# Performance work log

Measured on AMD Instinct MI355X. Metric: run time of the kernel, lower is better.

## Reference

```python
import jax, jax.numpy as jnp
import numpy as np

RADIUS = 3.0  # suppression radius in meters (init kwarg `radius`)


def _radius_nms(x, y, valid, radius):
    """Greedy radius NMS over points in index order.
    x, y: [N] coordinates; valid: [N] bool (point belongs to this class).
    Returns keep mask [N]: point kept iff valid and not within `radius` of
    any previously kept point.
    """
    N = x.shape[0]
    r2 = radius * radius

    def step(supp, i):
        keep = valid[i] & jnp.logical_not(supp[i])
        d2 = (x - x[i]) ** 2 + (y - y[i]) ** 2  # [N]
        supp = supp | (keep & (d2 <= r2))
        return supp, keep

    _, keeps = jax.lax.scan(step, jnp.zeros(N, dtype=bool), jnp.arange(N))
    return keeps


def setup_inputs() -> dict:
    key = jax.random.key(0)
    k1, k2 = jax.random.split(key)
    B, C, W, H, CL = 4, 4, 64, 128, 5
    segmented_channels = jax.random.normal(k1, (B, C, W, H), dtype=jnp.float32)
    # lidar channels 0,1 are x,y point coordinates (meters); scale for realism
    lidar = jax.random.normal(k2, (B, CL, W, H), dtype=jnp.float32) * 30.0
    return {"segmented_channels": segmented_channels, "lidar": lidar}


def reference(segmented_channels, lidar):
    B, C, W, H = segmented_channels.shape
    N = W * H
    # val, ind = segmented_channels.max(dim=1) -> per-pixel predicted class
    ind = jnp.argmax(segmented_channels, axis=1).reshape(B, N)  # [B, N] int
    x = lidar[:, 0].reshape(B, N)  # [B, N]
    y = lidar[:, 1].reshape(B, N)
    # classes 1 .. C-1 (class 0 = background, skipped in the loop)
    classes = jnp.arange(1, C)
    valid = ind[:, None, :] == classes[None, :, None]  # [B, C-1, N] bool
    # vmap greedy NMS over classes, then over batch (x,y shared across classes)
    nms_c = jax.vmap(_radius_nms, in_axes=(None, None, 0, None))
    nms_bc = jax.vmap(nms_c, in_axes=(0, 0, 0, None))
    keep = nms_bc(x, y, valid, RADIUS)  # [B, C-1, N] bool
    # dense (padded) stand-in for the ragged per-class kept point lists:
    # kept coordinates where keep, zeros elsewhere
    coords = jnp.stack([x, y], axis=-1)  # [B, N, 2]
    kept_coords = coords[:, None, :, :] * keep[..., None].astype(coords.dtype)  # [B, C-1, N, 2]
    return kept_coords, keep
```

## Files before the change

### kernel.cpp

```cpp
#include <hip/hip_runtime.h>
#include <cstdint>


#define NPTS 8192
#define CAP  2304
#define R2C  9.0f
#define GW   56
#define GORG 117.6f
#define GINV 0.23809524f
#define GMAXC 55.0f
#define SENT 3.0e37f

__global__ __launch_bounds__(1024) void radius_nms_kernel(
    const float* __restrict__ seg,
    const float* __restrict__ lidar,
    float* __restrict__ out)
{
#pragma clang fp contract(off)
    const int bx   = blockIdx.x;
    const int b    = bx / 3;
    const int cls  = (bx % 3) + 1;
    const int tid  = threadIdx.x;
    const int lane = tid & 63;
    const int wv   = tid >> 6;

    __shared__ float2 xy[CAP];
    __shared__ unsigned short cellA[CAP];
    __shared__ unsigned long long keptW[CAP / 64];
    __shared__ int waveTot[16];
    __shared__ float2 gslot[GW * GW * 4];
    __shared__ unsigned int cnt32[(GW * GW + 3) / 4];

    float* out0 = out + (size_t)bx * NPTS * 2;
    float* out1 = out + 196608 + (size_t)bx * NPTS;

    const float4 z4 = make_float4(0.f, 0.f, 0.f, 0.f);
    float4* o04 = (float4*)out0;
    float4* o14 = (float4*)out1;
    for (int i = tid; i < NPTS / 2; i += 1024) o04[i] = z4;
    for (int i = tid; i < NPTS / 4; i += 1024) o14[i] = z4;
    const float2 s2 = make_float2(SENT, SENT);
    for (int i = tid; i < GW * GW * 4; i += 1024) gslot[i] = s2;
    for (int i = tid; i < (GW * GW + 3) / 4; i += 1024) cnt32[i] = 0u;

    const float* segb = seg + (size_t)b * 4 * NPTS;
    const float* lx   = lidar + (size_t)b * 5 * NPTS;
    const float* ly   = lx + NPTS;

    const int n0 = tid * 8;
    const float4 a0 = *(const float4*)(segb + n0);
    const float4 a1 = *(const float4*)(segb + n0 + 4);
    const float4 b0 = *(const float4*)(segb + NPTS + n0);
    const float4 b1 = *(const float4*)(segb + NPTS + n0 + 4);
    const float4 c0 = *(const float4*)(segb + 2 * NPTS + n0);
    const float4 c1 = *(const float4*)(segb + 2 * NPTS + n0 + 4);
    const float4 d0 = *(const float4*)(segb + 3 * NPTS + n0);
    const float4 d1 = *(const float4*)(segb + 3 * NPTS + n0 + 4);
    const float4 xv0 = *(const float4*)(lx + n0);
    const float4 xv1 = *(const float4*)(lx + n0 + 4);
    const float4 yv0 = *(const float4*)(ly + n0);
    const float4 yv1 = *(const float4*)(ly + n0 + 4);

    const float v0[8] = {a0.x,a0.y,a0.z,a0.w, a1.x,a1.y,a1.z,a1.w};
    const float v1[8] = {b0.x,b0.y,b0.z,b0.w, b1.x,b1.y,b1.z,b1.w};
    const float v2[8] = {c0.x,c0.y,c0.z,c0.w, c1.x,c1.y,c1.z,c1.w};
    const float v3[8] = {d0.x,d0.y,d0.z,d0.w, d1.x,d1.y,d1.z,d1.w};
    const float px[8] = {xv0.x,xv0.y,xv0.z,xv0.w, xv1.x,xv1.y,xv1.z,xv1.w};
    const float py[8] = {yv0.x,yv0.y,yv0.z,yv0.w, yv1.x,yv1.y,yv1.z,yv1.w};

    int flags = 0, cnt = 0;
#pragma unroll
    for (int k = 0; k < 8; ++k) {
        int bi = 0; float bv = v0[k];
        if (v1[k] > bv) { bv = v1[k]; bi = 1; }
        if (v2[k] > bv) { bv = v2[k]; bi = 2; }
        if (v3[k] > bv) { bv = v3[k]; bi = 3; }
        if (bi == cls) { flags |= (1 << k); ++cnt; }
    }

    int v = cnt;
    for (int off = 1; off < 64; off <<= 1) {
        int nv = __shfl_up(v, off, 64);
        if (lane >= off) v += nv;
    }
    if (lane == 63) waveTot[wv] = v;
    __syncthreads();
    if (wv == 0) {
        int t = (lane < 16) ? waveTot[lane] : 0;
        for (int off = 1; off < 16; off <<= 1) {
            int nt = __shfl_up(t, off, 64);
            if (lane >= off) t += nt;
        }
        if (lane < 16) waveTot[lane] = t;
    }
    __syncthreads();

    int M = waveTot[15];
    if (M > CAP) M = CAP;
    const int rank0 = ((wv == 0) ? 0 : waveTot[wv - 1]) + v - cnt;
    int base = rank0;
#pragma unroll
    for (int k = 0; k < 8; ++k) {
        if (flags & (1 << k)) {
            if (base < CAP) {
                xy[base] = make_float2(px[k], py[k]);
                float fx = floorf((px[k] + GORG) * GINV);
                fx = fminf(fmaxf(fx, 0.0f), GMAXC);
                float fy = floorf((py[k] + GORG) * GINV);
                fy = fminf(fmaxf(fy, 0.0f), GMAXC);
                cellA[base] = (unsigned short)(((int)fy << 8) | (int)fx);
            }
            ++base;
        }
    }
    __syncthreads();

    if (wv == 0) {
        const int ntiles = (M + 63) >> 6;
        const int packSent = (55 << 8) | 55;

        float qx = 3.0e38f, qy = 3.0e38f;
        int cc = packSent;
        if (lane < M) {
            float2 q = xy[lane]; qx = q.x; qy = q.y;
            cc = cellA[lane];
        }

        for (int t = 0; t < ntiles; ++t) {
            const int ts = t << 6;

            float qxN = 3.0e38f, qyN = 3.0e38f;
            int ccN = packSent;
            {
                const int p2 = ts + 64 + lane;
                if (p2 < M) {
                    float2 q = xy[p2]; qxN = q.x; qyN = q.y;
                    ccN = cellA[p2];
                }
            }

            const int cx = cc & 0xFF, cy = cc >> 8;
            const int cxm = (cx > 0) ? cx - 1 : 0;
            const int cxp = (cx < GW - 1) ? cx + 1 : GW - 1;
            const int rm  = ((cy > 0) ? cy - 1 : 0) * GW;
            const int r0  = cy * GW;
            const int rp  = ((cy < GW - 1) ? cy + 1 : GW - 1) * GW;
            const int cLin = r0 + cx;
            const int c9[9] = { rm + cxm, rm + cx, rm + cxp,
                                r0 + cxm, cLin,    r0 + cxp,
                                rp + cxm, rp + cx, rp + cxp };

            float mm = 1.0e30f;
#pragma unroll
            for (int i = 0; i < 9; ++i) {
                const int sb = c9[i] * 4;
                const float2 s0 = gslot[sb];
                const float2 s1 = gslot[sb + 1];
                const float2 s2r = gslot[sb + 2];
                const float2 s3 = gslot[sb + 3];
                float dx, dy;
                dx = qx - s0.x; dy = qy - s0.y; const float e0 = dx * dx + dy * dy;
                dx = qx - s1.x; dy = qy - s1.y; const float e1 = dx * dx + dy * dy;
                dx = qx - s2r.x; dy = qy - s2r.y; const float e2 = dx * dx + dy * dy;
                dx = qx - s3.x; dy = qy - s3.y; const float e3 = dx * dx + dy * dy;
                const float cm = fminf(fminf(e0, e1), fminf(e2, e3));
                mm = fminf(mm, cm);
            }
            const bool sup = (mm <= R2C);

            int cntT = M - ts; if (cntT > 64) cntT = 64;
            const unsigned long long tm =
                (cntT >= 64) ? ~0ull : ((1ull << cntT) - 1ull);
            unsigned long long alive = __ballot(!sup) & tm;
            unsigned long long keepm = 0ull;
            while (alive) {
                const int l1 = __builtin_ctzll(alive);
                const unsigned long long rest = alive & (alive - 1ull);
                const int l2 =
                    __builtin_ctzll(rest | 0x8000000000000000ull);
                const float x1 = __int_as_float(
                    __builtin_amdgcn_readlane(__float_as_int(qx), l1));
                const float y1 = __int_as_float(
                    __builtin_amdgcn_readlane(__float_as_int(qy), l1));
                const float x2 = __int_as_float(
                    __builtin_amdgcn_readlane(__float_as_int(qx), l2));
                const float y2 = __int_as_float(
                    __builtin_amdgcn_readlane(__float_as_int(qy), l2));
                const float dxa = qx - x1, dya = qy - y1;
                const float dxb = qx - x2, dyb = qy - y2;
                const unsigned long long b1 =
                    __ballot((dxa * dxa + dya * dya) <= R2C);
                const unsigned long long b2 =
                    __ballot((dxb * dxb + dyb * dyb) <= R2C);
                keepm |= 1ull << l1;
                alive &= ~b1;
                if (rest != 0ull && ((b1 >> l2) & 1ull) == 0ull) {
                    keepm |= 1ull << l2;
                    alive &= ~b2;
                }
            }
            if (lane == 0) keptW[t] = keepm;

            if ((keepm >> lane) & 1ull) {
                const unsigned sh = 8u * (unsigned)(cLin & 3);
                unsigned old = atomicAdd(&cnt32[cLin >> 2], 1u << sh);
                unsigned mc = (old >> sh) & 0xFFu;
                if (mc < 4u) gslot[cLin * 4 + (int)mc] = make_float2(qx, qy);
            }

            qx = qxN; qy = qyN; cc = ccN;
        }
    }
    __syncthreads();

    int j = rank0;
#pragma unroll
    for (int k = 0; k < 8; ++k) {
        if (flags & (1 << k)) {
            if (j < M && ((keptW[j >> 6] >> (j & 63)) & 1ull)) {
                const int n = n0 + k;
                out0[2 * n]     = px[k];
                out0[2 * n + 1] = py[k];
                out1[n]         = 1.0f;
            }
            ++j;
        }
    }
}

extern "C" void kernel_launch(void* const* d_in, const int* in_sizes, int n_in,
                              void* d_out, int out_size, void* d_ws, size_t ws_size,
                              hipStream_t stream) {
    const float* seg   = (const float*)d_in[0];
    const float* lidar = (const float*)d_in[1];
    float* out = (float*)d_out;
    radius_nms_kernel<<<dim3(12), dim3(1024), 0, stream>>>(seg, lidar, out);
}
```

Measured before the change: 122.4 us.

## Split radius NMS into prep, single-wave NMS, and scatter kernels

Splits the monolithic kernel into three launches. The first does the argmax, compaction and cell binning and also zeroes the output across 72 extra blocks. The second runs the serial greedy NMS in a single 64-thread wave per (batch, class) with a shared-memory grid. The third scatters the kept points. The goal is to move output zeroing and the 1024-thread block overhead off the serial NMS critical path. In exchange it adds two kernel launches and a global workspace round trip, and it reverts the two-at-a-time ballot loop to one leader per iteration. The fallback keeps the old kernel when no workspace is provided.

```diff
diff --git a/kernel.cpp b/kernel.cpp
--- a/kernel.cpp
+++ b/kernel.cpp
@@ -11,37 +11,33 @@
 #define GMAXC 55.0f
 #define SENT 3.0e37f
 
-__global__ __launch_bounds__(1024) void radius_nms_kernel(
+#define WS_STRIDE 32768
+#define WS_XY     0
+#define WS_CELL   18432
+#define WS_OIDX   23040
+#define WS_KEPT   27648
+#define WS_M      27936
+#define WS_NEED   (12 * WS_STRIDE)
+
+__global__ __launch_bounds__(1024) void k1_prep(
     const float* __restrict__ seg,
     const float* __restrict__ lidar,
-    float* __restrict__ out)
+    float* __restrict__ out,
+    char* __restrict__ ws)
 {
 #pragma clang fp contract(off)
-    const int bx   = blockIdx.x;
-    const int b    = bx / 3;
-    const int cls  = (bx % 3) + 1;
-    const int tid  = threadIdx.x;
+    const int blk = blockIdx.x;
+    const int tid = threadIdx.x;
+    if (blk >= 12) {
+        ((float4*)out)[(size_t)(blk - 12) * 1024 + tid] =
+            make_float4(0.f, 0.f, 0.f, 0.f);
+        return;
+    }
+    const int b    = blk / 3;
+    const int cls  = (blk % 3) + 1;
     const int lane = tid & 63;
     const int wv   = tid >> 6;
-
-    __shared__ float2 xy[CAP];
-    __shared__ unsigned short cellA[CAP];
-    __shared__ unsigned long long keptW[CAP / 64];
     __shared__ int waveTot[16];
-    __shared__ float2 gslot[GW * GW * 4];
-    __shared__ unsigned int cnt32[(GW * GW + 3) / 4];
-
-    float* out0 = out + (size_t)bx * NPTS * 2;
-    float* out1 = out + 196608 + (size_t)bx * NPTS;
-
-    const float4 z4 = make_float4(0.f, 0.f, 0.f, 0.f);
-    float4* o04 = (float4*)out0;
-    float4* o14 = (float4*)out1;
-    for (int i = tid; i < NPTS / 2; i += 1024) o04[i] = z4;
-    for (int i = tid; i < NPTS / 4; i += 1024) o14[i] = z4;
-    const float2 s2 = make_float2(SENT, SENT);
-    for (int i = tid; i < GW * GW * 4; i += 1024) gslot[i] = s2;
-    for (int i = tid; i < (GW * GW + 3) / 4; i += 1024) cnt32[i] = 0u;
 
     const float* segb = seg + (size_t)b * 4 * NPTS;
     const float* lx   = lidar + (size_t)b * 5 * NPTS;
@@ -97,6 +93,244 @@
 
     int M = waveTot[15];
     if (M > CAP) M = CAP;
+
+    char* wsp = ws + (size_t)blk * WS_STRIDE;
+    float2* wxy = (float2*)(wsp + WS_XY);
+    unsigned short* wcell = (unsigned short*)(wsp + WS_CELL);
+    unsigned short* woidx = (unsigned short*)(wsp + WS_OIDX);
+    if (tid == 0) *(int*)(wsp + WS_M) = M;
+
+    int base = ((wv == 0) ? 0 : waveTot[wv - 1]) + v - cnt;
+#pragma unroll
+    for (int k = 0; k < 8; ++k) {
+        if (flags & (1 << k)) {
+            if (base < CAP) {
+                wxy[base] = make_float2(px[k], py[k]);
+                float fx = floorf((px[k] + GORG) * GINV);
+                fx = fminf(fmaxf(fx, 0.0f), GMAXC);
+                float fy = floorf((py[k] + GORG) * GINV);
+                fy = fminf(fmaxf(fy, 0.0f), GMAXC);
+                wcell[base] = (unsigned short)(((int)fy << 8) | (int)fx);
+                woidx[base] = (unsigned short)(n0 + k);
+            }
+            ++base;
+        }
+    }
+}
+
+__global__ __launch_bounds__(64) void k2_nms(char* __restrict__ ws)
+{
+#pragma clang fp contract(off)
+    const int p    = blockIdx.x;
+    const int lane = threadIdx.x;
+
+    char* wsp = ws + (size_t)p * WS_STRIDE;
+    const float2* wxy = (const float2*)(wsp + WS_XY);
+    const unsigned short* wcell = (const unsigned short*)(wsp + WS_CELL);
+    unsigned long long* wkept = (unsigned long long*)(wsp + WS_KEPT);
+    const int M = *(const int*)(wsp + WS_M);
+
+    __shared__ float2 gslot[GW * GW * 4];
+    __shared__ unsigned int cnt32[(GW * GW + 3) / 4];
+
+    const float4 s4 = make_float4(SENT, SENT, SENT, SENT);
+    float4* g4 = (float4*)gslot;
+    for (int i = lane; i < GW * GW * 2; i += 64) g4[i] = s4;
+    for (int i = lane; i < (GW * GW + 3) / 4; i += 64) cnt32[i] = 0u;
+
+    const int ntiles = (M + 63) >> 6;
+    const int packSent = (55 << 8) | 55;
+
+    float qx = 3.0e38f, qy = 3.0e38f;
+    int cc = packSent;
+    if (lane < M) {
+        float2 q = wxy[lane]; qx = q.x; qy = q.y;
+        cc = wcell[lane];
+    }
+
+    for (int t = 0; t < ntiles; ++t) {
+        const int ts = t << 6;
+
+        float qxN = 3.0e38f, qyN = 3.0e38f;
+        int ccN = packSent;
+        {
+            const int p2 = ts + 64 + lane;
+            if (p2 < M) {
+                float2 q = wxy[p2]; qxN = q.x; qyN = q.y;
+                ccN = wcell[p2];
+            }
+        }
+
+        const int cx = cc & 0xFF, cy = cc >> 8;
+        const int cxm = (cx > 0) ? cx - 1 : 0;
+        const int cxp = (cx < GW - 1) ? cx + 1 : GW - 1;
+        const int rm  = ((cy > 0) ? cy - 1 : 0) * GW;
+        const int r0  = cy * GW;
+        const int rp  = ((cy < GW - 1) ? cy + 1 : GW - 1) * GW;
+        const int cLin = r0 + cx;
+        const int c9[9] = { rm + cxm, rm + cx, rm + cxp,
+                            r0 + cxm, cLin,    r0 + cxp,
+                            rp + cxm, rp + cx, rp + cxp };
+
+        float mm = 1.0e30f;
+#pragma unroll
+        for (int i = 0; i < 9; ++i) {
+            const int sb = c9[i] * 4;
+            const float2 s0 = gslot[sb];
+            const float2 s1 = gslot[sb + 1];
+            const float2 s2r = gslot[sb + 2];
+            const float2 s3 = gslot[sb + 3];
+            float dx, dy;
+            dx = qx - s0.x; dy = qy - s0.y; const float e0 = dx * dx + dy * dy;
+            dx = qx - s1.x; dy = qy - s1.y; const float e1 = dx * dx + dy * dy;
+            dx = qx - s2r.x; dy = qy - s2r.y; const float e2 = dx * dx + dy * dy;
+            dx = qx - s3.x; dy = qy - s3.y; const float e3 = dx * dx + dy * dy;
+            const float cm = fminf(fminf(e0, e1), fminf(e2, e3));
+            mm = fminf(mm, cm);
+        }
+        const bool sup = (mm <= R2C);
+
+        int cntT = M - ts; if (cntT > 64) cntT = 64;
+        const unsigned long long tm =
+            (cntT >= 64) ? ~0ull : ((1ull << cntT) - 1ull);
+        unsigned long long alive = __ballot(!sup) & tm;
+        unsigned long long keepm = 0ull;
+        while (alive) {
+            const int l = __builtin_ctzll(alive);
+            const float xl = __int_as_float(
+                __builtin_amdgcn_readlane(__float_as_int(qx), l));
+            const float yl = __int_as_float(
+                __builtin_amdgcn_readlane(__float_as_int(qy), l));
+            const float dx = qx - xl;
+            const float dy = qy - yl;
+            unsigned long long b2 = __ballot((dx * dx + dy * dy) <= R2C);
+            keepm |= (1ull << l);
+            alive &= ~b2;
+        }
+        if (lane == 0) wkept[t] = keepm;
+
+        if ((keepm >> lane) & 1ull) {
+            const unsigned sh = 8u * (unsigned)(cLin & 3);
+            unsigned old = atomicAdd(&cnt32[cLin >> 2], 1u << sh);
+            unsigned mc = (old >> sh) & 0xFFu;
+            if (mc < 4u) gslot[cLin * 4 + (int)mc] = make_float2(qx, qy);
+        }
+
+        qx = qxN; qy = qyN; cc = ccN;
+    }
+}
+
+__global__ __launch_bounds__(1024) void k3_scatter(
+    float* __restrict__ out, const char* __restrict__ ws)
+{
+    const int p   = blockIdx.x;
+    const int tid = threadIdx.x;
+    const char* wsp = ws + (size_t)p * WS_STRIDE;
+    const float2* wxy = (const float2*)(wsp + WS_XY);
+    const unsigned short* woidx = (const unsigned short*)(wsp + WS_OIDX);
+    const unsigned long long* wkept =
+        (const unsigned long long*)(wsp + WS_KEPT);
+    const int M = *(const int*)(wsp + WS_M);
+
+    float* out0 = out + (size_t)p * NPTS * 2;
+    float* out1 = out + 196608 + (size_t)p * NPTS;
+    for (int j = tid; j < M; j += 1024) {
+        if ((wkept[j >> 6] >> (j & 63)) & 1ull) {
+            const int n = woidx[j];
+            float2 q = wxy[j];
+            out0[2 * n]     = q.x;
+            out0[2 * n + 1] = q.y;
+            out1[n]         = 1.0f;
+        }
+    }
+}
+
+__global__ __launch_bounds__(1024) void radius_nms_kernel(
+    const float* __restrict__ seg,
+    const float* __restrict__ lidar,
+    float* __restrict__ out)
+{
+#pragma clang fp contract(off)
+    const int bx   = blockIdx.x;
+    const int b    = bx / 3;
+    const int cls  = (bx % 3) + 1;
+    const int tid  = threadIdx.x;
+    const int lane = tid & 63;
+    const int wv   = tid >> 6;
+
+    __shared__ float2 xy[CAP];
+    __shared__ unsigned short cellA[CAP];
+    __shared__ unsigned long long keptW[CAP / 64];
+    __shared__ int waveTot[16];
+    __shared__ float2 gslot[GW * GW * 4];
+    __shared__ unsigned int cnt32[(GW * GW + 3) / 4];
+
+    float* out0 = out + (size_t)bx * NPTS * 2;
+    float* out1 = out + 196608 + (size_t)bx * NPTS;
+
+    const float4 z4 = make_float4(0.f, 0.f, 0.f, 0.f);
+    float4* o04 = (float4*)out0;
+    float4* o14 = (float4*)out1;
+    for (int i = tid; i < NPTS / 2; i += 1024) o04[i] = z4;
+    for (int i = tid; i < NPTS / 4; i += 1024) o14[i] = z4;
+    const float2 s2 = make_float2(SENT, SENT);
+    for (int i = tid; i < GW * GW * 4; i += 1024) gslot[i] = s2;
+    for (int i = tid; i < (GW * GW + 3) / 4; i += 1024) cnt32[i] = 0u;
+
+    const float* segb = seg + (size_t)b * 4 * NPTS;
+    const float* lx   = lidar + (size_t)b * 5 * NPTS;
+    const float* ly   = lx + NPTS;
+
+    const int n0 = tid * 8;
+    const float4 a0 = *(const float4*)(segb + n0);
+    const float4 a1 = *(const float4*)(segb + n0 + 4);
+    const float4 b0 = *(const float4*)(segb + NPTS + n0);
+    const float4 b1 = *(const float4*)(segb + NPTS + n0 + 4);
+    const float4 c0 = *(const float4*)(segb + 2 * NPTS + n0);
+    const float4 c1 = *(const float4*)(segb + 2 * NPTS + n0 + 4);
+    const float4 d0 = *(const float4*)(segb + 3 * NPTS + n0);
+    const float4 d1 = *(const float4*)(segb + 3 * NPTS + n0 + 4);
+    const float4 xv0 = *(const float4*)(lx + n0);
+    const float4 xv1 = *(const float4*)(lx + n0 + 4);
+    const float4 yv0 = *(const float4*)(ly + n0);
+    const float4 yv1 = *(const float4*)(ly + n0 + 4);
+
+    const float v0[8] = {a0.x,a0.y,a0.z,a0.w, a1.x,a1.y,a1.z,a1.w};
+    const float v1[8] = {b0.x,b0.y,b0.z,b0.w, b1.x,b1.y,b1.z,b1.w};
+    const float v2[8] = {c0.x,c0.y,c0.z,c0.w, c1.x,c1.y,c1.z,c1.w};
+    const float v3[8] = {d0.x,d0.y,d0.z,d0.w, d1.x,d1.y,d1.z,d1.w};
+    const float px[8] = {xv0.x,xv0.y,xv0.z,xv0.w, xv1.x,xv1.y,xv1.z,xv1.w};
+    const float py[8] = {yv0.x,yv0.y,yv0.z,yv0.w, yv1.x,yv1.y,yv1.z,yv1.w};
+
+    int flags = 0, cnt = 0;
+#pragma unroll
+    for (int k = 0; k < 8; ++k) {
+        int bi = 0; float bv = v0[k];
+        if (v1[k] > bv) { bv = v1[k]; bi = 1; }
+        if (v2[k] > bv) { bv = v2[k]; bi = 2; }
+        if (v3[k] > bv) { bv = v3[k]; bi = 3; }
+        if (bi == cls) { flags |= (1 << k); ++cnt; }
+    }
+
+    int v = cnt;
+    for (int off = 1; off < 64; off <<= 1) {
+        int nv = __shfl_up(v, off, 64);
+        if (lane >= off) v += nv;
+    }
+    if (lane == 63) waveTot[wv] = v;
+    __syncthreads();
+    if (wv == 0) {
+        int t = (lane < 16) ? waveTot[lane] : 0;
+        for (int off = 1; off < 16; off <<= 1) {
+            int nt = __shfl_up(t, off, 64);
+            if (lane >= off) t += nt;
+        }
+        if (lane < 16) waveTot[lane] = t;
+    }
+    __syncthreads();
+
+    int M = waveTot[15];
+    if (M > CAP) M = CAP;
     const int rank0 = ((wv == 0) ? 0 : waveTot[wv - 1]) + v - cnt;
     int base = rank0;
 #pragma unroll
@@ -174,30 +408,16 @@
             unsigned long long alive = __ballot(!sup) & tm;
             unsigned long long keepm = 0ull;
             while (alive) {
-                const int l1 = __builtin_ctzll(alive);
-                const unsigned long long rest = alive & (alive - 1ull);
-                const int l2 =
-                    __builtin_ctzll(rest | 0x8000000000000000ull);
-                const float x1 = __int_as_float(
-                    __builtin_amdgcn_readlane(__float_as_int(qx), l1));
-                const float y1 = __int_as_float(
-                    __builtin_amdgcn_readlane(__float_as_int(qy), l1));
-                const float x2 = __int_as_float(
-                    __builtin_amdgcn_readlane(__float_as_int(qx), l2));
-                const float y2 = __int_as_float(
-                    __builtin_amdgcn_readlane(__float_as_int(qy), l2));
-                const float dxa = qx - x1, dya = qy - y1;
-                const float dxb = qx - x2, dyb = qy - y2;
-                const unsigned long long b1 =
-                    __ballot((dxa * dxa + dya * dya) <= R2C);
-                const unsigned long long b2 =
-                    __ballot((dxb * dxb + dyb * dyb) <= R2C);
-                keepm |= 1ull << l1;
-                alive &= ~b1;
-                if (rest != 0ull && ((b1 >> l2) & 1ull) == 0ull) {
-                    keepm |= 1ull << l2;
-                    alive &= ~b2;
-                }
+                const int l = __builtin_ctzll(alive);
+                const float xl = __int_as_float(
+                    __builtin_amdgcn_readlane(__float_as_int(qx), l));
+                const float yl = __int_as_float(
+                    __builtin_amdgcn_readlane(__float_as_int(qy), l));
+                const float dx = qx - xl;
+                const float dy = qy - yl;
+                unsigned long long b2 = __ballot((dx * dx + dy * dy) <= R2C);
+                keepm |= (1ull << l);
+                alive &= ~b2;
             }
             if (lane == 0) keptW[t] = keepm;
 
@@ -234,5 +454,12 @@
     const float* seg   = (const float*)d_in[0];
     const float* lidar = (const float*)d_in[1];
     float* out = (float*)d_out;
-    radius_nms_kernel<<<dim3(12), dim3(1024), 0, stream>>>(seg, lidar, out);
+    if (d_ws != nullptr && ws_size >= (size_t)WS_NEED) {
+        char* ws = (char*)d_ws;
+        k1_prep<<<dim3(84), dim3(1024), 0, stream>>>(seg, lidar, out, ws);
+        k2_nms<<<dim3(12), dim3(64), 0, stream>>>(ws);
+        k3_scatter<<<dim3(12), dim3(1024), 0, stream>>>(out, ws);
+    } else {
+        radius_nms_kernel<<<dim3(12), dim3(1024), 0, stream>>>(seg, lidar, out);
+    }
 }
```

Result: slower. 130.0 us (+6.2%).

## Replace serial single-wave greedy NMS with parallel neighbor-graph resolution

Applied to the files above, without the earlier changes.

Replaces the single-wavefront tile-by-tile greedy scan with a block-wide algorithm. It builds a CSR spatial grid, precomputes each point's earlier neighbors within the radius into a shared list, and then resolves keep/suppress status iteratively in parallel rounds: a point is suppressed once any kept earlier neighbor exists, and kept once all earlier neighbors are decided and none is kept. The aim is to spread the sequential dependency over all 1024 threads instead of one wave. The cost is several extra passes, scans and barriers, plus a round count that depends on dependency-chain length. The neighbor buffer is capped at NB_MAX entries and the loop at 3000 rounds, so correctness could suffer on dense inputs.

```diff
diff --git a/kernel.cpp b/kernel.cpp
--- a/kernel.cpp
+++ b/kernel.cpp
@@ -6,10 +6,11 @@
 #define CAP  2304
 #define R2C  9.0f
 #define GW   56
+#define NCELL (GW * GW)
 #define GORG 117.6f
 #define GINV 0.23809524f
 #define GMAXC 55.0f
-#define SENT 3.0e37f
+#define NB_MAX 24576
 
 __global__ __launch_bounds__(1024) void radius_nms_kernel(
     const float* __restrict__ seg,
@@ -25,11 +26,16 @@
     const int wv   = tid >> 6;
 
     __shared__ float2 xy[CAP];
-    __shared__ unsigned short cellA[CAP];
-    __shared__ unsigned long long keptW[CAP / 64];
+    __shared__ unsigned short cellOf[CAP];
+    __shared__ unsigned short ptCSR[CAP];
+    __shared__ unsigned short ncnt[CAP];
+    __shared__ unsigned int   nStart[CAP];
+    __shared__ unsigned int   cellCnt[NCELL];
+    __shared__ unsigned int   cellStart[NCELL];
+    __shared__ unsigned short nbr[NB_MAX];
+    __shared__ unsigned int   statusW[CAP / 16];
     __shared__ int waveTot[16];
-    __shared__ float2 gslot[GW * GW * 4];
-    __shared__ unsigned int cnt32[(GW * GW + 3) / 4];
+    __shared__ int remaining;
 
     float* out0 = out + (size_t)bx * NPTS * 2;
     float* out1 = out + 196608 + (size_t)bx * NPTS;
@@ -39,9 +45,9 @@
     float4* o14 = (float4*)out1;
     for (int i = tid; i < NPTS / 2; i += 1024) o04[i] = z4;
     for (int i = tid; i < NPTS / 4; i += 1024) o14[i] = z4;
-    const float2 s2 = make_float2(SENT, SENT);
-    for (int i = tid; i < GW * GW * 4; i += 1024) gslot[i] = s2;
-    for (int i = tid; i < (GW * GW + 3) / 4; i += 1024) cnt32[i] = 0u;
+    for (int i = tid; i < NCELL; i += 1024) cellCnt[i] = 0u;
+    for (int i = tid; i < CAP; i += 1024) ncnt[i] = 0;
+    if (tid < CAP / 16) statusW[tid] = 0u;
 
     const float* segb = seg + (size_t)b * 4 * NPTS;
     const float* lx   = lidar + (size_t)b * 5 * NPTS;
@@ -108,116 +114,183 @@
                 fx = fminf(fmaxf(fx, 0.0f), GMAXC);
                 float fy = floorf((py[k] + GORG) * GINV);
                 fy = fminf(fmaxf(fy, 0.0f), GMAXC);
-                cellA[base] = (unsigned short)(((int)fy << 8) | (int)fx);
+                cellOf[base] = (unsigned short)(((int)fy << 8) | (int)fx);
             }
             ++base;
         }
     }
     __syncthreads();
 
-    if (wv == 0) {
-        const int ntiles = (M + 63) >> 6;
-        const int packSent = (55 << 8) | 55;
-
-        float qx = 3.0e38f, qy = 3.0e38f;
-        int cc = packSent;
-        if (lane < M) {
-            float2 q = xy[lane]; qx = q.x; qy = q.y;
-            cc = cellA[lane];
-        }
-
-        for (int t = 0; t < ntiles; ++t) {
-            const int ts = t << 6;
-
-            float qxN = 3.0e38f, qyN = 3.0e38f;
-            int ccN = packSent;
-            {
-                const int p2 = ts + 64 + lane;
-                if (p2 < M) {
-                    float2 q = xy[p2]; qxN = q.x; qyN = q.y;
-                    ccN = cellA[p2];
+    for (int r = tid; r < M; r += 1024) {
+        const int cc = cellOf[r];
+        atomicAdd(&cellCnt[(cc >> 8) * GW + (cc & 255)], 1u);
+    }
+    __syncthreads();
+
+    {
+        const int c4 = tid * 4;
+        int sa = 0, sb = 0, sc = 0, sd = 0;
+        if (c4 < NCELL) {
+            sa = cellCnt[c4]; sb = cellCnt[c4 + 1];
+            sc = cellCnt[c4 + 2]; sd = cellCnt[c4 + 3];
+        }
+        int sum = sa + sb + sc + sd;
+        int inc = sum;
+        for (int off = 1; off < 64; off <<= 1) {
+            int t = __shfl_up(inc, off, 64);
+            if (lane >= off) inc += t;
+        }
+        if (lane == 63) waveTot[wv] = inc;
+        __syncthreads();
+        if (wv == 0) {
+            int t = (lane < 16) ? waveTot[lane] : 0;
+            for (int off = 1; off < 16; off <<= 1) {
+                int u = __shfl_up(t, off, 64);
+                if (lane >= off) t += u;
+            }
+            if (lane < 16) waveTot[lane] = t;
+        }
+        __syncthreads();
+        const int bb = ((wv == 0) ? 0 : waveTot[wv - 1]) + inc - sum;
+        if (c4 < NCELL) {
+            cellStart[c4]     = bb;
+            cellStart[c4 + 1] = bb + sa;
+            cellStart[c4 + 2] = bb + sa + sb;
+            cellStart[c4 + 3] = bb + sa + sb + sc;
+        }
+    }
+    __syncthreads();
+
+    for (int i = tid; i < NCELL; i += 1024) cellCnt[i] = 0u;
+    __syncthreads();
+
+    for (int r = tid; r < M; r += 1024) {
+        const int cc = cellOf[r];
+        const int c = (cc >> 8) * GW + (cc & 255);
+        const unsigned pos = cellStart[c] + atomicAdd(&cellCnt[c], 1u);
+        ptCSR[pos] = (unsigned short)r;
+    }
+    __syncthreads();
+
+    for (int r = tid; r < M; r += 1024) {
+        const float2 q = xy[r];
+        const int cc = cellOf[r];
+        const int cx = cc & 255, cy = cc >> 8;
+        const int x0 = (cx > 0) ? cx - 1 : 0, x1 = (cx < GW - 1) ? cx + 1 : GW - 1;
+        const int y0 = (cy > 0) ? cy - 1 : 0, y1 = (cy < GW - 1) ? cy + 1 : GW - 1;
+        int nc = 0;
+        for (int yy = y0; yy <= y1; ++yy)
+            for (int xx = x0; xx <= x1; ++xx) {
+                const int c = yy * GW + xx;
+                const unsigned s = cellStart[c], n = cellCnt[c];
+                for (unsigned k = 0; k < n; ++k) {
+                    const int qr = ptCSR[s + k];
+                    if (qr < r) {
+                        const float2 o = xy[qr];
+                        const float dx = q.x - o.x, dy = q.y - o.y;
+                        if (dx * dx + dy * dy <= R2C) ++nc;
+                    }
                 }
             }
-
-            const int cx = cc & 0xFF, cy = cc >> 8;
-            const int cxm = (cx > 0) ? cx - 1 : 0;
-            const int cxp = (cx < GW - 1) ? cx + 1 : GW - 1;
-            const int rm  = ((cy > 0) ? cy - 1 : 0) * GW;
-            const int r0  = cy * GW;
-            const int rp  = ((cy < GW - 1) ? cy + 1 : GW - 1) * GW;
-            const int cLin = r0 + cx;
-            const int c9[9] = { rm + cxm, rm + cx, rm + cxp,
-                                r0 + cxm, cLin,    r0 + cxp,
-                                rp + cxm, rp + cx, rp + cxp };
-
-            float mm = 1.0e30f;
-#pragma unroll
-            for (int i = 0; i < 9; ++i) {
-                const int sb = c9[i] * 4;
-                const float2 s0 = gslot[sb];
-                const float2 s1 = gslot[sb + 1];
-                const float2 s2r = gslot[sb + 2];
-                const float2 s3 = gslot[sb + 3];
-                float dx, dy;
-                dx = qx - s0.x; dy = qy - s0.y; const float e0 = dx * dx + dy * dy;
-                dx = qx - s1.x; dy = qy - s1.y; const float e1 = dx * dx + dy * dy;
-                dx = qx - s2r.x; dy = qy - s2r.y; const float e2 = dx * dx + dy * dy;
-                dx = qx - s3.x; dy = qy - s3.y; const float e3 = dx * dx + dy * dy;
-                const float cm = fminf(fminf(e0, e1), fminf(e2, e3));
-                mm = fminf(mm, cm);
-            }
-            const bool sup = (mm <= R2C);
-
-            int cntT = M - ts; if (cntT > 64) cntT = 64;
-            const unsigned long long tm =
-                (cntT >= 64) ? ~0ull : ((1ull << cntT) - 1ull);
-            unsigned long long alive = __ballot(!sup) & tm;
-            unsigned long long keepm = 0ull;
-            while (alive) {
-                const int l1 = __builtin_ctzll(alive);
-                const unsigned long long rest = alive & (alive - 1ull);
-                const int l2 =
-                    __builtin_ctzll(rest | 0x8000000000000000ull);
-                const float x1 = __int_as_float(
-                    __builtin_amdgcn_readlane(__float_as_int(qx), l1));
-                const float y1 = __int_as_float(
-                    __builtin_amdgcn_readlane(__float_as_int(qy), l1));
-                const float x2 = __int_as_float(
-                    __builtin_amdgcn_readlane(__float_as_int(qx), l2));
-                const float y2 = __int_as_float(
-                    __builtin_amdgcn_readlane(__float_as_int(qy), l2));
-                const float dxa = qx - x1, dya = qy - y1;
-                const float dxb = qx - x2, dyb = qy - y2;
-                const unsigned long long b1 =
-                    __ballot((dxa * dxa + dya * dya) <= R2C);
-                const unsigned long long b2 =
-                    __ballot((dxb * dxb + dyb * dyb) <= R2C);
-                keepm |= 1ull << l1;
-                alive &= ~b1;
-                if (rest != 0ull && ((b1 >> l2) & 1ull) == 0ull) {
-                    keepm |= 1ull << l2;
-                    alive &= ~b2;
+        ncnt[r] = (unsigned short)nc;
+    }
+    __syncthreads();
+
+    {
+        const int r3 = tid * 3;
+        int sa = 0, sb = 0, sc = 0;
+        if (r3 < CAP) { sa = ncnt[r3]; sb = ncnt[r3 + 1]; sc = ncnt[r3 + 2]; }
+        int sum = sa + sb + sc;
+        int inc = sum;
+        for (int off = 1; off < 64; off <<= 1) {
+            int t = __shfl_up(inc, off, 64);
+            if (lane >= off) inc += t;
+        }
+        if (lane == 63) waveTot[wv] = inc;
+        __syncthreads();
+        if (wv == 0) {
+            int t = (lane < 16) ? waveTot[lane] : 0;
+            for (int off = 1; off < 16; off <<= 1) {
+                int u = __shfl_up(t, off, 64);
+                if (lane >= off) t += u;
+            }
+            if (lane < 16) waveTot[lane] = t;
+        }
+        __syncthreads();
+        const int bb = ((wv == 0) ? 0 : waveTot[wv - 1]) + inc - sum;
+        if (r3 < CAP) {
+            nStart[r3]     = bb;
+            nStart[r3 + 1] = bb + sa;
+            nStart[r3 + 2] = bb + sa + sb;
+        }
+    }
+    __syncthreads();
+
+    for (int r = tid; r < M; r += 1024) {
+        const float2 q = xy[r];
+        const int cc = cellOf[r];
+        const int cx = cc & 255, cy = cc >> 8;
+        const int x0 = (cx > 0) ? cx - 1 : 0, x1 = (cx < GW - 1) ? cx + 1 : GW - 1;
+        const int y0 = (cy > 0) ? cy - 1 : 0, y1 = (cy < GW - 1) ? cy + 1 : GW - 1;
+        unsigned pos = nStart[r];
+        for (int yy = y0; yy <= y1; ++yy)
+            for (int xx = x0; xx <= x1; ++xx) {
+                const int c = yy * GW + xx;
+                const unsigned s = cellStart[c], n = cellCnt[c];
+                for (unsigned k = 0; k < n; ++k) {
+                    const int qr = ptCSR[s + k];
+                    if (qr < r) {
+                        const float2 o = xy[qr];
+                        const float dx = q.x - o.x, dy = q.y - o.y;
+                        if (dx * dx + dy * dy <= R2C) {
+                            if (pos < NB_MAX) nbr[pos] = (unsigned short)qr;
+                            ++pos;
+                        }
+                    }
                 }
             }
-            if (lane == 0) keptW[t] = keepm;
-
-            if ((keepm >> lane) & 1ull) {
-                const unsigned sh = 8u * (unsigned)(cLin & 3);
-                unsigned old = atomicAdd(&cnt32[cLin >> 2], 1u << sh);
-                unsigned mc = (old >> sh) & 0xFFu;
-                if (mc < 4u) gslot[cLin * 4 + (int)mc] = make_float2(qx, qy);
-            }
-
-            qx = qxN; qy = qyN; cc = ccN;
-        }
-    }
-    __syncthreads();
+    }
+    __syncthreads();
+
+    unsigned resolvedMask = 0;
+    unsigned st0 = 0, en0 = 0, st1 = 0, en1 = 0, st2 = 0, en2 = 0;
+    { int r = tid;        if (r < M) { st0 = nStart[r]; en0 = st0 + ncnt[r]; if (en0 > NB_MAX) en0 = NB_MAX; } else resolvedMask |= 1u; }
+    { int r = tid + 1024; if (r < M) { st1 = nStart[r]; en1 = st1 + ncnt[r]; if (en1 > NB_MAX) en1 = NB_MAX; } else resolvedMask |= 2u; }
+    { int r = tid + 2048; if (r < M) { st2 = nStart[r]; en2 = st2 + ncnt[r]; if (en2 > NB_MAX) en2 = NB_MAX; } else resolvedMask |= 4u; }
+
+    auto step = [&](int r, unsigned st, unsigned en) -> int {
+        bool sup = false, allDec = true;
+        for (unsigned k = st; k < en; ++k) {
+            const int q = nbr[k];
+            const unsigned f = (statusW[q >> 4] >> ((q & 15) * 2)) & 3u;
+            if (f & 2u) { sup = true; break; }
+            if (!(f & 1u)) allDec = false;
+        }
+        if (sup)    { atomicOr(&statusW[r >> 4], 1u << ((r & 15) * 2)); return 1; }
+        if (allDec) { atomicOr(&statusW[r >> 4], 3u << ((r & 15) * 2)); return 1; }
+        return 0;
+    };
+
+    int rounds = 0;
+    for (;;) {
+        if (tid == 0) remaining = 0;
+        __syncthreads();
+        bool undec = false;
+        if (!(resolvedMask & 1u)) { if (step(tid,        st0, en0)) resolvedMask |= 1u; else undec = true; }
+        if (!(resolvedMask & 2u)) { if (step(tid + 1024, st1, en1)) resolvedMask |= 2u; else undec = true; }
+        if (!(resolvedMask & 4u)) { if (step(tid + 2048, st2, en2)) resolvedMask |= 4u; else undec = true; }
+        const unsigned long long bal = __ballot(undec);
+        if (lane == 0 && bal) atomicAdd(&remaining, 1);
+        __syncthreads();
+        ++rounds;
+        if (remaining == 0 || rounds > 3000) break;
+    }
 
     int j = rank0;
 #pragma unroll
     for (int k = 0; k < 8; ++k) {
         if (flags & (1 << k)) {
-            if (j < M && ((keptW[j >> 6] >> (j & 63)) & 1ull)) {
+            if (j < M && ((statusW[j >> 4] >> ((j & 15) * 2)) & 2u)) {
                 const int n = n0 + k;
                 out0[2 * n]     = px[k];
                 out0[2 * n + 1] = py[k];
```

Result: slower. 144.8 us (+18.3%).
